# Kernel tuning notes

Measured on AMD Instinct MI355X. Metric: run time of the kernel, lower is better.

The kernel has to match this reference:

```python
import jax, jax.numpy as jnp
import numpy as np

B, T, D = 2, 2048, 2048
H = 16
SEM_HD, GEO_HD = 64, 64
SEM_D, GEO_D = H * SEM_HD, H * GEO_HD  # 1024, 1024
V_D = 2048
V_HD = V_D // H  # 128
ROPE_BASE = 10000.0
NEG_INF = -1e9


def _shape(x, hd):
    # (B, T, H*hd) -> (B, H, T, hd)
    b, t, _ = x.shape
    return x.reshape(b, t, H, hd).transpose(0, 2, 1, 3)


def _rope(x, pos_offset=0):
    # half-split (Llama-style) rotary on last dim; x: (B, H, T, hd)
    hd = x.shape[-1]
    half = hd // 2
    inv_freq = 1.0 / (ROPE_BASE ** (jnp.arange(0, half, dtype=jnp.float32) / half))
    pos = jnp.arange(x.shape[2], dtype=jnp.float32) + pos_offset
    ang = pos[:, None] * inv_freq[None, :]            # (T, half)
    cos, sin = jnp.cos(ang), jnp.sin(ang)
    x1, x2 = x[..., :half], x[..., half:]
    return jnp.concatenate([x1 * cos - x2 * sin, x2 * cos + x1 * sin], axis=-1).astype(x.dtype)


def setup_inputs() -> dict:
    key = jax.random.key(0)
    ks = jax.random.split(key, 9)
    s = lambda fan_in: 1.0 / np.sqrt(fan_in)
    return {
        "x": jax.random.normal(ks[0], (B, T, D), dtype=jnp.float32),
        "w_q_sem": jax.random.normal(ks[1], (D, SEM_D), dtype=jnp.float32) * s(D),
        "w_k_sem": jax.random.normal(ks[2], (D, SEM_D), dtype=jnp.float32) * s(D),
        "w_q_geo": jax.random.normal(ks[3], (D, GEO_D), dtype=jnp.float32) * s(D),
        "w_k_geo": jax.random.normal(ks[4], (D, GEO_D), dtype=jnp.float32) * s(D),
        "w_v": jax.random.normal(ks[5], (D, V_D), dtype=jnp.float32) * s(D),
        "w_out": jax.random.normal(ks[6], (V_D, D), dtype=jnp.float32) * s(V_D),
        "gate_logit": jax.random.normal(ks[7], (H,), dtype=jnp.float32) * 0.1,
        "gate_w": jax.random.normal(ks[8], (D, H), dtype=jnp.float32) * 0.01,
    }


def reference(x, w_q_sem, w_k_sem, w_q_geo, w_k_geo, w_v, w_out, gate_logit, gate_w):
    sem_scale = 1.0 / np.sqrt(float(SEM_HD))
    geo_scale = 1.0 / np.sqrt(float(GEO_HD))

    qs = _shape(x @ w_q_sem, SEM_HD)   # (B,H,T,sem_hd)
    ks = _shape(x @ w_k_sem, SEM_HD)
    qg = _shape(x @ w_q_geo, GEO_HD)   # (B,H,T,geo_hd)
    kg = _shape(x @ w_k_geo, GEO_HD)
    vh = _shape(x @ w_v, V_HD)         # (B,H,T,v_hd)

    # RoPE only on geometric dims
    qg = _rope(qg)
    kg = _rope(kg)

    sem_scores = jnp.einsum("bhtd,bhsd->bhts", qs, ks) * sem_scale
    geo_scores = jnp.einsum("bhtd,bhsd->bhts", qg, kg) * geo_scale

    # per-head gate: static logit + dynamic projection of x, sigmoid in fp32
    dyn = (x @ gate_w).transpose(0, 2, 1)[..., None]            # (B,H,T,1)
    gate = jax.nn.sigmoid(gate_logit[None, :, None, None] + dyn)
    scores = gate * sem_scores + (1.0 - gate) * geo_scores      # (B,H,T,S)

    causal = jnp.tril(jnp.ones((T, T), dtype=bool))
    scores = jnp.where(causal[None, None], scores, NEG_INF)
    attn = jax.nn.softmax(scores, axis=-1)

    out = jnp.einsum("bhts,bhsd->bhtd", attn, vh)               # (B,H,T,v_hd)
    y = out.transpose(0, 2, 1, 3).reshape(B, T, V_D) @ w_out    # (B,T,D)
    return y
```

## Files before the change

kernel.cpp:

```cpp
#include <hip/hip_runtime.h>
#include <hip/hip_bf16.h>
#include <math.h>

#define B_ 2
#define T_ 2048
#define D_ 2048
#define H_ 16

typedef __attribute__((ext_vector_type(8))) short bf16x8;
typedef __attribute__((ext_vector_type(4))) float f32x4;
typedef unsigned short ushort_t;

__device__ __forceinline__ ushort_t f2bf(float f) {
    unsigned int u = __float_as_uint(f);
    u += 0x7fffu + ((u >> 16) & 1u);
    return (ushort_t)(u >> 16);
}

__device__ __forceinline__ void gl_lds16(const void* g, void* l) {
    __builtin_amdgcn_global_load_lds(
        (const __attribute__((address_space(1))) void*)g,
        (__attribute__((address_space(3))) void*)l, 16, 0, 0);
}

__global__ __launch_bounds__(256) void cvt_bf16(
    const float* __restrict__ in, ushort_t* __restrict__ out)
{
    const int base = (blockIdx.x * 256 + threadIdx.x) * 8;
    const float4 a = *(const float4*)(in + base);
    const float4 b = *(const float4*)(in + base + 4);
    unsigned int r0 = (unsigned int)f2bf(a.x) | ((unsigned int)f2bf(a.y) << 16);
    unsigned int r1 = (unsigned int)f2bf(a.z) | ((unsigned int)f2bf(a.w) << 16);
    unsigned int r2 = (unsigned int)f2bf(b.x) | ((unsigned int)f2bf(b.y) << 16);
    unsigned int r3 = (unsigned int)f2bf(b.z) | ((unsigned int)f2bf(b.w) << 16);
    *(uint4*)(out + base) = make_uint4(r0, r1, r2, r3);
}

__global__ __launch_bounds__(256) void cvt_tr_bf16(
    const float* __restrict__ in, ushort_t* __restrict__ out, int K, int N)
{
    __shared__ float t[64][65];
    const int n0 = blockIdx.x * 64, k0 = blockIdx.y * 64;
    const int tx = threadIdx.x & 63, ty = threadIdx.x >> 6;
#pragma unroll
    for (int i = 0; i < 16; i++) {
        const int r = i * 4 + ty;
        t[r][tx] = in[(size_t)(k0 + r) * N + n0 + tx];
    }
    __syncthreads();
#pragma unroll
    for (int i = 0; i < 16; i++) {
        const int nn = i * 4 + ty;
        out[(size_t)(n0 + nn) * K + k0 + tx] = f2bf(t[tx][nn]);
    }
}

__device__ __forceinline__ void gemm_core(
    const ushort_t* __restrict__ Ab, const ushort_t* __restrict__ BTb,
    int K, int row0, int col0,
    ushort_t* As, ushort_t* Bs, f32x4 (&acc)[4][4], int w, int lane)
{
    const int lm = lane & 15, lk = (lane >> 4) << 3;
    const int wr = w >> 1, wc = w & 1;
#pragma unroll
    for (int m = 0; m < 4; m++)
#pragma unroll
        for (int n = 0; n < 4; n++) {
            acc[m][n][0] = 0.f; acc[m][n][1] = 0.f;
            acc[m][n][2] = 0.f; acc[m][n][3] = 0.f;
        }

    for (int k0 = 0; k0 < K; k0 += 32) {
        __syncthreads();
#pragma unroll
        for (int i = 0; i < 2; i++) {
            const int chunk = i * 4 + w;
            const int idx = chunk * 64 + lane;
            const int r = idx >> 2;
            const int c = (idx & 3) << 3;
            gl_lds16(Ab + (size_t)(row0 + r) * K + k0 + c, As + chunk * 512);
            gl_lds16(BTb + (size_t)(col0 + r) * K + k0 + c, Bs + chunk * 512);
        }
        __syncthreads();

        bf16x8 av[4], bv[4];
#pragma unroll
        for (int m = 0; m < 4; m++)
            av[m] = *(const bf16x8*)&As[(wr * 64 + m * 16 + lm) * 32 + lk];
#pragma unroll
        for (int n = 0; n < 4; n++)
            bv[n] = *(const bf16x8*)&Bs[(wc * 64 + n * 16 + lm) * 32 + lk];
#pragma unroll
        for (int m = 0; m < 4; m++)
#pragma unroll
            for (int n = 0; n < 4; n++)
                acc[m][n] = __builtin_amdgcn_mfma_f32_16x16x32_bf16(
                    av[m], bv[n], acc[m][n], 0, 0, 0);
    }
}

__device__ __forceinline__ void xcd_tile(int& row0, int& col0)
{
    const int o = blockIdx.y * gridDim.x + blockIdx.x;
    const int nwg = gridDim.x * gridDim.y;
    const int s = (o & 7) * (nwg >> 3) + (o >> 3);
    col0 = (s % gridDim.x) << 7;
    row0 = (s / gridDim.x) << 7;
}

__global__ __launch_bounds__(256) void gemm_bf16_bt(
    const ushort_t* __restrict__ Ab, const ushort_t* __restrict__ BTb,
    float* __restrict__ C, int N, int K)
{
    __shared__ ushort_t As[4096];
    __shared__ ushort_t Bs[4096];
    const int tid = threadIdx.x;
    const int w = tid >> 6, lane = tid & 63;
    int row0, col0;
    xcd_tile(row0, col0);
    f32x4 acc[4][4];
    gemm_core(Ab, BTb, K, row0, col0, As, Bs, acc, w, lane);

    const int wr = w >> 1, wc = w & 1;
    const int lm = lane & 15;
#pragma unroll
    for (int m = 0; m < 4; m++) {
        const int rowb = row0 + wr * 64 + m * 16 + ((lane >> 4) << 2);
#pragma unroll
        for (int n = 0; n < 4; n++) {
            const int col = col0 + wc * 64 + n * 16 + lm;
#pragma unroll
            for (int r = 0; r < 4; r++)
                C[(size_t)(rowb + r) * N + col] = acc[m][n][r];
        }
    }
}

__global__ __launch_bounds__(256) void gemm_bf16_bf16out(
    const ushort_t* __restrict__ Ab, const ushort_t* __restrict__ BTb,
    ushort_t* __restrict__ C, int N, int K)
{
    __shared__ ushort_t As[4096];
    __shared__ ushort_t Bs[4096];
    const int tid = threadIdx.x;
    const int w = tid >> 6, lane = tid & 63;
    int row0, col0;
    xcd_tile(row0, col0);
    f32x4 acc[4][4];
    gemm_core(Ab, BTb, K, row0, col0, As, Bs, acc, w, lane);

    const int wr = w >> 1, wc = w & 1;
    const int lm = lane & 15;
#pragma unroll
    for (int m = 0; m < 4; m++) {
        const int rowb = row0 + wr * 64 + m * 16 + ((lane >> 4) << 2);
#pragma unroll
        for (int n = 0; n < 4; n++) {
            const int col = col0 + wc * 64 + n * 16 + lm;
#pragma unroll
            for (int r = 0; r < 4; r++)
                C[(size_t)(rowb + r) * N + col] = f2bf(acc[m][n][r]);
        }
    }
}

__global__ __launch_bounds__(256) void gemm_qk_fused(
    const ushort_t* __restrict__ Ab, const ushort_t* __restrict__ BTb,
    const float* __restrict__ GATE, const float2* __restrict__ tab,
    ushort_t* __restrict__ Qb, ushort_t* __restrict__ Kb, int K)
{
    __shared__ ushort_t As[4096];
    __shared__ ushort_t Bs[4096];
    const int tid = threadIdx.x;
    const int w = tid >> 6, lane = tid & 63;
    int row0, col0;
    xcd_tile(row0, col0);
    f32x4 acc[4][4];
    gemm_core(Ab, BTb, K, row0, col0, As, Bs, acc, w, lane);

    const int wr = w >> 1, wc = w & 1;
    const int lm = lane & 15, lg = lane >> 4;
    const int col_base = col0 + wc * 64;
    const int region = col_base >> 10;
    const int h = (col_base >> 6) & 15;

#pragma unroll
    for (int m = 0; m < 4; m++) {
        const int rbase = row0 + wr * 64 + m * 16 + (lg << 2);
#pragma unroll
        for (int r = 0; r < 4; r++) {
            const int row = rbase + r;
            const int t = row & (T_ - 1);
            const int bq = row >> 11;
            const size_t obase = ((size_t)(bq * 16 + h) * 2048 + t) * 128;
            if (region == 0) {
                const float sc = GATE[row * 16 + h] * 0.125f;
#pragma unroll
                for (int n = 0; n < 4; n++)
                    Qb[obase + n * 16 + lm] = f2bf(acc[m][n][r] * sc);
            } else if (region == 1) {
                const int sw = (t & 7) << 3;
#pragma unroll
                for (int n = 0; n < 4; n++)
                    Kb[obase + ((n * 16 + lm) ^ sw)] = f2bf(acc[m][n][r]);
            } else if (region == 2) {
                const float sc = (1.f - GATE[row * 16 + h]) * 0.125f;
#pragma unroll
                for (int n = 0; n < 2; n++) {
                    const int j = n * 16 + lm;
                    const float2 cs = tab[t * 32 + j];
                    const float x1 = acc[m][n][r], x2 = acc[m][n + 2][r];
                    Qb[obase + 64 + j] = f2bf((x1 * cs.x - x2 * cs.y) * sc);
                    Qb[obase + 96 + j] = f2bf((x2 * cs.x + x1 * cs.y) * sc);
                }
            } else {
                const int sw = (t & 7) << 3;
#pragma unroll
                for (int n = 0; n < 2; n++) {
                    const int j = n * 16 + lm;
                    const float2 cs = tab[t * 32 + j];
                    const float x1 = acc[m][n][r], x2 = acc[m][n + 2][r];
                    Kb[obase + ((64 + j) ^ sw)] = f2bf(x1 * cs.x - x2 * cs.y);
                    Kb[obase + ((96 + j) ^ sw)] = f2bf(x2 * cs.x + x1 * cs.y);
                }
            }
        }
    }
}

__global__ __launch_bounds__(256) void gate_kernel(
    const float* __restrict__ x, const float* __restrict__ gw,
    const float* __restrict__ glogit, float* __restrict__ gate)
{
    __shared__ float xs[2048];
    __shared__ float red[256];
    const int row = blockIdx.x, tid = threadIdx.x;
#pragma unroll
    for (int i = 0; i < 8; i++) xs[i * 256 + tid] = x[(size_t)row * 2048 + i * 256 + tid];
    __syncthreads();
    const int h = tid & 15, chunk = tid >> 4;
    float acc = 0.f;
#pragma unroll 4
    for (int d0 = 0; d0 < 128; d0++) {
        const int d = chunk * 128 + d0;
        acc += xs[d] * gw[d * 16 + h];
    }
    red[tid] = acc;
    __syncthreads();
    for (int st = 8; st >= 1; st >>= 1) {
        if (chunk < st) red[chunk * 16 + h] += red[(chunk + st) * 16 + h];
        __syncthreads();
    }
    if (tid < 16) gate[row * 16 + tid] = 1.f / (1.f + expf(-(glogit[tid] + red[tid])));
}

__global__ __launch_bounds__(256) void rope_table(float2* __restrict__ tab)
{
    const int gid = blockIdx.x * 256 + threadIdx.x;
    const int j = gid & 31, t = gid >> 5;
    const float invf = exp2f((float)j * -0.41524101186091903f);
    const float ang = (float)t * invf;
    tab[gid] = make_float2(cosf(ang), sinf(ang));
}

__global__ __launch_bounds__(256) void prep_v(
    const ushort_t* __restrict__ Vbb, ushort_t* __restrict__ Vt)
{
    __shared__ ushort_t tile[64][65];
    const int t0 = blockIdx.x * 64, dv0 = blockIdx.y * 64, bh = blockIdx.z;
    const int b = bh >> 4, h = bh & 15;
    const int c = threadIdx.x & 63, rq = threadIdx.x >> 6;
#pragma unroll
    for (int i = 0; i < 16; i++) {
        const int r = i * 4 + rq;
        tile[r][c] = Vbb[(size_t)(b * T_ + t0 + r) * 2048 + h * 128 + dv0 + c];
    }
    __syncthreads();
#pragma unroll
    for (int i = 0; i < 16; i++) {
        const int dvr = i * 4 + rq;
        const int dv = dv0 + dvr;
        Vt[((size_t)bh * 128 + dv) * 2048 + t0 + (c ^ ((dv & 7) << 3))] = tile[c][dvr];
    }
}

__global__ __launch_bounds__(256, 2) void attn_mfma(
    const ushort_t* __restrict__ Qb, const ushort_t* __restrict__ Kb,
    const ushort_t* __restrict__ Vt, ushort_t* __restrict__ OUT)
{
    __shared__ ushort_t Ks[64 * 128];
    __shared__ ushort_t Vs[128 * 64];
    __shared__ ushort_t Ps[4][32 * 72];

    const int tid = threadIdx.x;
    const int w = tid >> 6, l = tid & 63;
    const int lg = l >> 4, lm = l & 15;
    const int bh = blockIdx.y;
    const int t0 = (gridDim.x - 1 - blockIdx.x) << 7;
    const size_t hb = (size_t)bh * 2048 * 128;

    bf16x8 qf[2][4];
#pragma unroll
    for (int m = 0; m < 2; m++)
#pragma unroll
        for (int ks = 0; ks < 4; ks++)
            qf[m][ks] = *(const bf16x8*)(Qb + hb +
                (size_t)(t0 + w * 32 + m * 16 + lm) * 128 + ks * 32 + lg * 8);

    f32x4 o[2][8];
    float mi[2][4], li[2][4];
#pragma unroll
    for (int m = 0; m < 2; m++) {
#pragma unroll
        for (int r = 0; r < 4; r++) { mi[m][r] = -1e30f; li[m][r] = 0.f; }
#pragma unroll
        for (int nv = 0; nv < 8; nv++) {
            o[m][nv][0] = 0.f; o[m][nv][1] = 0.f; o[m][nv][2] = 0.f; o[m][nv][3] = 0.f;
        }
    }

    ushort_t* pw = &Ps[w][0];
    const int nkt = (t0 >> 6) + 2;

    for (int kt = 0; kt < nkt; kt++) {
        const int s0 = kt << 6;
        __syncthreads();
#pragma unroll
        for (int rr = 0; rr < 4; rr++) {
            const int chunk = rr * 4 + w;
            gl_lds16(Kb + hb + (size_t)(s0 + chunk * 4 + lg) * 128 + lm * 8,
                     Ks + chunk * 512);
        }
#pragma unroll
        for (int rr = 0; rr < 4; rr++) {
            const int chunk = rr * 4 + w;
            gl_lds16(Vt + hb + (size_t)(chunk * 8 + (l >> 3)) * 2048 + s0 + (l & 7) * 8,
                     Vs + chunk * 512);
        }
        __syncthreads();

        f32x4 sacc[2][4];
#pragma unroll
        for (int m = 0; m < 2; m++)
#pragma unroll
            for (int n = 0; n < 4; n++) {
                sacc[m][n][0] = 0.f; sacc[m][n][1] = 0.f;
                sacc[m][n][2] = 0.f; sacc[m][n][3] = 0.f;
            }
#pragma unroll
        for (int ks = 0; ks < 4; ks++) {
            bf16x8 bfr[4];
#pragma unroll
            for (int n = 0; n < 4; n++) {
                const int key = n * 16 + lm;
                const int d = ks * 32 + lg * 8;
                bfr[n] = *(const bf16x8*)&Ks[key * 128 + (d ^ ((key & 7) << 3))];
            }
#pragma unroll
            for (int m = 0; m < 2; m++)
#pragma unroll
                for (int n = 0; n < 4; n++)
                    sacc[m][n] = __builtin_amdgcn_mfma_f32_16x16x32_bf16(
                        qf[m][ks], bfr[n], sacc[m][n], 0, 0, 0);
        }

        if (kt >= nkt - 2) {
#pragma unroll
            for (int m = 0; m < 2; m++)
#pragma unroll
                for (int n = 0; n < 4; n++)
#pragma unroll
                    for (int r = 0; r < 4; r++) {
                        const int rowt = t0 + w * 32 + m * 16 + lg * 4 + r;
                        const int colt = s0 + n * 16 + lm;
                        if (colt > rowt) sacc[m][n][r] = -1e30f;
                    }
        }

#pragma unroll
        for (int m = 0; m < 2; m++) {
#pragma unroll
            for (int r = 0; r < 4; r++) {
                float mt = fmaxf(fmaxf(sacc[m][0][r], sacc[m][1][r]),
                                 fmaxf(sacc[m][2][r], sacc[m][3][r]));
                mt = fmaxf(mt, __shfl_xor(mt, 1));
                mt = fmaxf(mt, __shfl_xor(mt, 2));
                mt = fmaxf(mt, __shfl_xor(mt, 4));
                mt = fmaxf(mt, __shfl_xor(mt, 8));
                const float mnew = fmaxf(mi[m][r], mt);
                const float alpha = __expf(mi[m][r] - mnew);
                float rs = 0.f;
#pragma unroll
                for (int n = 0; n < 4; n++) {
                    const float p = __expf(sacc[m][n][r] - mnew);
                    sacc[m][n][r] = p;
                    rs += p;
                }
                rs += __shfl_xor(rs, 1);
                rs += __shfl_xor(rs, 2);
                rs += __shfl_xor(rs, 4);
                rs += __shfl_xor(rs, 8);
                li[m][r] = li[m][r] * alpha + rs;
                mi[m][r] = mnew;
#pragma unroll
                for (int nv = 0; nv < 8; nv++) o[m][nv][r] *= alpha;
#pragma unroll
                for (int n = 0; n < 4; n++)
                    pw[(m * 16 + lg * 4 + r) * 72 + n * 16 + lm] = f2bf(sacc[m][n][r]);
            }
        }

#pragma unroll
        for (int ks2 = 0; ks2 < 2; ks2++) {
            bf16x8 pa[2];
#pragma unroll
            for (int m = 0; m < 2; m++)
                pa[m] = *(const bf16x8*)&pw[(m * 16 + lm) * 72 + ks2 * 32 + lg * 8];
#pragma unroll
            for (int nv = 0; nv < 8; nv++) {
                const int dv = nv * 16 + lm;
                const bf16x8 vb = *(const bf16x8*)&Vs[dv * 64 +
                    ((ks2 * 32 + lg * 8) ^ ((dv & 7) << 3))];
#pragma unroll
                for (int m = 0; m < 2; m++)
                    o[m][nv] = __builtin_amdgcn_mfma_f32_16x16x32_bf16(
                        pa[m], vb, o[m][nv], 0, 0, 0);
            }
        }
    }

    const int b = bh >> 4, h = bh & 15;
#pragma unroll
    for (int m = 0; m < 2; m++)
#pragma unroll
        for (int r = 0; r < 4; r++) {
            const float inv = 1.f / li[m][r];
            const int trow = t0 + w * 32 + m * 16 + lg * 4 + r;
            ushort_t* orow = OUT + (size_t)(b * T_ + trow) * 2048 + h * 128 + lm;
#pragma unroll
            for (int nv = 0; nv < 8; nv++)
                orow[nv * 16] = f2bf(o[m][nv][r] * inv);
        }
}

extern "C" void kernel_launch(void* const* d_in, const int* in_sizes, int n_in,
                              void* d_out, int out_size, void* d_ws, size_t ws_size,
                              hipStream_t stream)
{
    const float* x       = (const float*)d_in[0];
    const float* w_q_sem = (const float*)d_in[1];
    const float* w_k_sem = (const float*)d_in[2];
    const float* w_q_geo = (const float*)d_in[3];
    const float* w_k_geo = (const float*)d_in[4];
    const float* w_v     = (const float*)d_in[5];
    const float* w_out   = (const float*)d_in[6];
    const float* glogit  = (const float*)d_in[7];
    const float* gw      = (const float*)d_in[8];
    float* out = (float*)d_out;

    const int M = B_ * T_;
    const size_t MB8 = (size_t)8 * 1024 * 1024;

    ushort_t* xbf = (ushort_t*)d_ws;
    ushort_t* WT  = xbf + MB8;
    ushort_t* Qb  = WT + MB8;
    ushort_t* Kb  = Qb + MB8;
    ushort_t* Vt  = Kb + MB8;
    ushort_t* Vbb = Vt + MB8;
    float* GATE   = (float*)(Vbb + MB8);
    float2* TAB   = (float2*)(GATE + 65536);
    ushort_t* ATTbf = Vbb;

    dim3 blk(256);

    cvt_bf16<<<dim3(M * 2048 / (256 * 8)), blk, 0, stream>>>(x, xbf);
    cvt_tr_bf16<<<dim3(16, 32), blk, 0, stream>>>(w_q_sem, WT + (size_t)0 * 2097152, 2048, 1024);
    cvt_tr_bf16<<<dim3(16, 32), blk, 0, stream>>>(w_k_sem, WT + (size_t)1 * 2097152, 2048, 1024);
    cvt_tr_bf16<<<dim3(16, 32), blk, 0, stream>>>(w_q_geo, WT + (size_t)2 * 2097152, 2048, 1024);
    cvt_tr_bf16<<<dim3(16, 32), blk, 0, stream>>>(w_k_geo, WT + (size_t)3 * 2097152, 2048, 1024);
    gate_kernel<<<dim3(M), blk, 0, stream>>>(x, gw, glogit, GATE);
    rope_table<<<dim3(256), blk, 0, stream>>>(TAB);

    gemm_qk_fused<<<dim3(32, 32), blk, 0, stream>>>(xbf, WT, GATE, TAB, Qb, Kb, 2048);

    cvt_tr_bf16<<<dim3(32, 32), blk, 0, stream>>>(w_v, WT, 2048, 2048);
    gemm_bf16_bf16out<<<dim3(16, 32), blk, 0, stream>>>(xbf, WT, Vbb, 2048, 2048);
    prep_v<<<dim3(T_ / 64, 2, 32), blk, 0, stream>>>(Vbb, Vt);

    attn_mfma<<<dim3(T_ / 128, 32), blk, 0, stream>>>(Qb, Kb, Vt, ATTbf);

    cvt_tr_bf16<<<dim3(32, 32), blk, 0, stream>>>(w_out, WT, 2048, 2048);
    gemm_bf16_bt<<<dim3(16, 32), blk, 0, stream>>>(ATTbf, WT, out, 2048, 2048);
}
```

Baseline: 552.2 us.

## Fuse prep kernels, pair causal tiles in attention, add lazy rescale and setprio

```diff
diff --git a/kernel.cpp b/kernel.cpp
--- a/kernel.cpp
+++ b/kernel.cpp
@@ -23,17 +23,49 @@
         (__attribute__((address_space(3))) void*)l, 16, 0, 0);
 }
 
-__global__ __launch_bounds__(256) void cvt_bf16(
-    const float* __restrict__ in, ushort_t* __restrict__ out)
-{
-    const int base = (blockIdx.x * 256 + threadIdx.x) * 8;
-    const float4 a = *(const float4*)(in + base);
-    const float4 b = *(const float4*)(in + base + 4);
+__global__ __launch_bounds__(256) void cvt_gate_kernel(
+    const float* __restrict__ x, const float* __restrict__ gw,
+    const float* __restrict__ glogit,
+    ushort_t* __restrict__ xbf, float* __restrict__ gate)
+{
+    __shared__ float xs[2048];
+    __shared__ float red[256];
+    const int row = blockIdx.x, tid = threadIdx.x;
+
+    const float4 a = *(const float4*)(x + (size_t)row * 2048 + tid * 8);
+    const float4 b = *(const float4*)(x + (size_t)row * 2048 + tid * 8 + 4);
     unsigned int r0 = (unsigned int)f2bf(a.x) | ((unsigned int)f2bf(a.y) << 16);
     unsigned int r1 = (unsigned int)f2bf(a.z) | ((unsigned int)f2bf(a.w) << 16);
     unsigned int r2 = (unsigned int)f2bf(b.x) | ((unsigned int)f2bf(b.y) << 16);
     unsigned int r3 = (unsigned int)f2bf(b.z) | ((unsigned int)f2bf(b.w) << 16);
-    *(uint4*)(out + base) = make_uint4(r0, r1, r2, r3);
+    *(uint4*)(xbf + (size_t)row * 2048 + tid * 8) = make_uint4(r0, r1, r2, r3);
+    *(float4*)&xs[tid * 8] = a;
+    *(float4*)&xs[tid * 8 + 4] = b;
+    __syncthreads();
+
+    const int h = tid & 15, chunk = tid >> 4;
+    float acc = 0.f;
+#pragma unroll 4
+    for (int d0 = 0; d0 < 128; d0++) {
+        const int d = chunk * 128 + d0;
+        acc += xs[d] * gw[d * 16 + h];
+    }
+    red[tid] = acc;
+    __syncthreads();
+    for (int st = 8; st >= 1; st >>= 1) {
+        if (chunk < st) red[chunk * 16 + h] += red[(chunk + st) * 16 + h];
+        __syncthreads();
+    }
+    if (tid < 16) gate[row * 16 + tid] = 1.f / (1.f + expf(-(glogit[tid] + red[tid])));
+}
+
+__global__ __launch_bounds__(256) void rope_table(float2* __restrict__ tab)
+{
+    const int gid = blockIdx.x * 256 + threadIdx.x;
+    const int j = gid & 31, t = gid >> 5;
+    const float invf = exp2f((float)j * -0.41524101186091903f);
+    const float ang = (float)t * invf;
+    tab[gid] = make_float2(cosf(ang), sinf(ang));
 }
 
 __global__ __launch_bounds__(256) void cvt_tr_bf16(
@@ -52,6 +84,31 @@
     for (int i = 0; i < 16; i++) {
         const int nn = i * 4 + ty;
         out[(size_t)(n0 + nn) * K + k0 + tx] = f2bf(t[tx][nn]);
+    }
+}
+
+__global__ __launch_bounds__(256) void cvt_tr4_bf16(
+    const float* __restrict__ s0, const float* __restrict__ s1,
+    const float* __restrict__ s2, const float* __restrict__ s3,
+    ushort_t* __restrict__ out)
+{
+    __shared__ float t[64][65];
+    const int z = blockIdx.z;
+    const float* in = (z == 0) ? s0 : (z == 1) ? s1 : (z == 2) ? s2 : s3;
+    ushort_t* o = out + (size_t)z * 2097152;
+    const int N = 1024, K = 2048;
+    const int n0 = blockIdx.x * 64, k0 = blockIdx.y * 64;
+    const int tx = threadIdx.x & 63, ty = threadIdx.x >> 6;
+#pragma unroll
+    for (int i = 0; i < 16; i++) {
+        const int r = i * 4 + ty;
+        t[r][tx] = in[(size_t)(k0 + r) * N + n0 + tx];
+    }
+    __syncthreads();
+#pragma unroll
+    for (int i = 0; i < 16; i++) {
+        const int nn = i * 4 + ty;
+        o[(size_t)(n0 + nn) * K + k0 + tx] = f2bf(t[tx][nn]);
     }
 }
 
@@ -90,12 +147,14 @@
 #pragma unroll
         for (int n = 0; n < 4; n++)
             bv[n] = *(const bf16x8*)&Bs[(wc * 64 + n * 16 + lm) * 32 + lk];
+        __builtin_amdgcn_s_setprio(1);
 #pragma unroll
         for (int m = 0; m < 4; m++)
 #pragma unroll
             for (int n = 0; n < 4; n++)
                 acc[m][n] = __builtin_amdgcn_mfma_f32_16x16x32_bf16(
                     av[m], bv[n], acc[m][n], 0, 0, 0);
+        __builtin_amdgcn_s_setprio(0);
     }
 }
 
@@ -228,41 +287,6 @@
     }
 }
 
-__global__ __launch_bounds__(256) void gate_kernel(
-    const float* __restrict__ x, const float* __restrict__ gw,
-    const float* __restrict__ glogit, float* __restrict__ gate)
-{
-    __shared__ float xs[2048];
-    __shared__ float red[256];
-    const int row = blockIdx.x, tid = threadIdx.x;
-#pragma unroll
-    for (int i = 0; i < 8; i++) xs[i * 256 + tid] = x[(size_t)row * 2048 + i * 256 + tid];
-    __syncthreads();
-    const int h = tid & 15, chunk = tid >> 4;
-    float acc = 0.f;
-#pragma unroll 4
-    for (int d0 = 0; d0 < 128; d0++) {
-        const int d = chunk * 128 + d0;
-        acc += xs[d] * gw[d * 16 + h];
-    }
-    red[tid] = acc;
-    __syncthreads();
-    for (int st = 8; st >= 1; st >>= 1) {
-        if (chunk < st) red[chunk * 16 + h] += red[(chunk + st) * 16 + h];
-        __syncthreads();
-    }
-    if (tid < 16) gate[row * 16 + tid] = 1.f / (1.f + expf(-(glogit[tid] + red[tid])));
-}
-
-__global__ __launch_bounds__(256) void rope_table(float2* __restrict__ tab)
-{
-    const int gid = blockIdx.x * 256 + threadIdx.x;
-    const int j = gid & 31, t = gid >> 5;
-    const float invf = exp2f((float)j * -0.41524101186091903f);
-    const float ang = (float)t * invf;
-    tab[gid] = make_float2(cosf(ang), sinf(ang));
-}
-
 __global__ __launch_bounds__(256) void prep_v(
     const ushort_t* __restrict__ Vbb, ushort_t* __restrict__ Vt)
 {
@@ -296,151 +320,164 @@
     const int w = tid >> 6, l = tid & 63;
     const int lg = l >> 4, lm = l & 15;
     const int bh = blockIdx.y;
-    const int t0 = (gridDim.x - 1 - blockIdx.x) << 7;
+    const int pair = blockIdx.x;
     const size_t hb = (size_t)bh * 2048 * 128;
-
-    bf16x8 qf[2][4];
-#pragma unroll
-    for (int m = 0; m < 2; m++)
-#pragma unroll
-        for (int ks = 0; ks < 4; ks++)
-            qf[m][ks] = *(const bf16x8*)(Qb + hb +
-                (size_t)(t0 + w * 32 + m * 16 + lm) * 128 + ks * 32 + lg * 8);
-
-    f32x4 o[2][8];
-    float mi[2][4], li[2][4];
-#pragma unroll
-    for (int m = 0; m < 2; m++) {
-#pragma unroll
-        for (int r = 0; r < 4; r++) { mi[m][r] = -1e30f; li[m][r] = 0.f; }
-#pragma unroll
-        for (int nv = 0; nv < 8; nv++) {
-            o[m][nv][0] = 0.f; o[m][nv][1] = 0.f; o[m][nv][2] = 0.f; o[m][nv][3] = 0.f;
-        }
-    }
-
+    const int b = bh >> 4, h = bh & 15;
     ushort_t* pw = &Ps[w][0];
-    const int nkt = (t0 >> 6) + 2;
-
-    for (int kt = 0; kt < nkt; kt++) {
-        const int s0 = kt << 6;
-        __syncthreads();
-#pragma unroll
-        for (int rr = 0; rr < 4; rr++) {
-            const int chunk = rr * 4 + w;
-            gl_lds16(Kb + hb + (size_t)(s0 + chunk * 4 + lg) * 128 + lm * 8,
-                     Ks + chunk * 512);
-        }
-#pragma unroll
-        for (int rr = 0; rr < 4; rr++) {
-            const int chunk = rr * 4 + w;
-            gl_lds16(Vt + hb + (size_t)(chunk * 8 + (l >> 3)) * 2048 + s0 + (l & 7) * 8,
-                     Vs + chunk * 512);
-        }
-        __syncthreads();
-
-        f32x4 sacc[2][4];
+
+    for (int half = 0; half < 2; half++) {
+        const int tile = (half == 0) ? (15 - pair) : pair;
+        const int t0 = tile << 7;
+
+        bf16x8 qf[2][4];
 #pragma unroll
         for (int m = 0; m < 2; m++)
 #pragma unroll
-            for (int n = 0; n < 4; n++) {
-                sacc[m][n][0] = 0.f; sacc[m][n][1] = 0.f;
-                sacc[m][n][2] = 0.f; sacc[m][n][3] = 0.f;
-            }
-#pragma unroll
-        for (int ks = 0; ks < 4; ks++) {
-            bf16x8 bfr[4];
-#pragma unroll
-            for (int n = 0; n < 4; n++) {
-                const int key = n * 16 + lm;
-                const int d = ks * 32 + lg * 8;
-                bfr[n] = *(const bf16x8*)&Ks[key * 128 + (d ^ ((key & 7) << 3))];
-            }
+            for (int ks = 0; ks < 4; ks++)
+                qf[m][ks] = *(const bf16x8*)(Qb + hb +
+                    (size_t)(t0 + w * 32 + m * 16 + lm) * 128 + ks * 32 + lg * 8);
+
+        f32x4 o[2][8];
+        float mi[2][4], li[2][4];
+#pragma unroll
+        for (int m = 0; m < 2; m++) {
+#pragma unroll
+            for (int r = 0; r < 4; r++) { mi[m][r] = -1e30f; li[m][r] = 0.f; }
+#pragma unroll
+            for (int nv = 0; nv < 8; nv++) {
+                o[m][nv][0] = 0.f; o[m][nv][1] = 0.f;
+                o[m][nv][2] = 0.f; o[m][nv][3] = 0.f;
+            }
+        }
+
+        const int nkt = 2 * tile + 2;
+        for (int kt = 0; kt < nkt; kt++) {
+            const int s0 = kt << 6;
+            __syncthreads();
+#pragma unroll
+            for (int rr = 0; rr < 4; rr++) {
+                const int chunk = rr * 4 + w;
+                gl_lds16(Kb + hb + (size_t)(s0 + chunk * 4 + lg) * 128 + lm * 8,
+                         Ks + chunk * 512);
+            }
+#pragma unroll
+            for (int rr = 0; rr < 4; rr++) {
+                const int chunk = rr * 4 + w;
+                gl_lds16(Vt + hb + (size_t)(chunk * 8 + (l >> 3)) * 2048 + s0 + (l & 7) * 8,
+                         Vs + chunk * 512);
+            }
+            __syncthreads();
+
+            f32x4 sacc[2][4];
 #pragma unroll
             for (int m = 0; m < 2; m++)
 #pragma unroll
-                for (int n = 0; n < 4; n++)
-                    sacc[m][n] = __builtin_amdgcn_mfma_f32_16x16x32_bf16(
-                        qf[m][ks], bfr[n], sacc[m][n], 0, 0, 0);
-        }
-
-        if (kt >= nkt - 2) {
-#pragma unroll
-            for (int m = 0; m < 2; m++)
-#pragma unroll
-                for (int n = 0; n < 4; n++)
-#pragma unroll
-                    for (int r = 0; r < 4; r++) {
-                        const int rowt = t0 + w * 32 + m * 16 + lg * 4 + r;
-                        const int colt = s0 + n * 16 + lm;
-                        if (colt > rowt) sacc[m][n][r] = -1e30f;
+                for (int n = 0; n < 4; n++) {
+                    sacc[m][n][0] = 0.f; sacc[m][n][1] = 0.f;
+                    sacc[m][n][2] = 0.f; sacc[m][n][3] = 0.f;
+                }
+#pragma unroll
+            for (int ks = 0; ks < 4; ks++) {
+                bf16x8 bfr[4];
+#pragma unroll
+                for (int n = 0; n < 4; n++) {
+                    const int key = n * 16 + lm;
+                    const int d = ks * 32 + lg * 8;
+                    bfr[n] = *(const bf16x8*)&Ks[key * 128 + (d ^ ((key & 7) << 3))];
+                }
+                __builtin_amdgcn_s_setprio(1);
+#pragma unroll
+                for (int m = 0; m < 2; m++)
+#pragma unroll
+                    for (int n = 0; n < 4; n++)
+                        sacc[m][n] = __builtin_amdgcn_mfma_f32_16x16x32_bf16(
+                            qf[m][ks], bfr[n], sacc[m][n], 0, 0, 0);
+                __builtin_amdgcn_s_setprio(0);
+            }
+
+            if (kt >= nkt - 2) {
+#pragma unroll
+                for (int m = 0; m < 2; m++)
+#pragma unroll
+                    for (int n = 0; n < 4; n++)
+#pragma unroll
+                        for (int r = 0; r < 4; r++) {
+                            const int rowt = t0 + w * 32 + m * 16 + lg * 4 + r;
+                            const int colt = s0 + n * 16 + lm;
+                            if (colt > rowt) sacc[m][n][r] = -1e30f;
+                        }
+            }
+
+#pragma unroll
+            for (int m = 0; m < 2; m++) {
+#pragma unroll
+                for (int r = 0; r < 4; r++) {
+                    float mt = fmaxf(fmaxf(sacc[m][0][r], sacc[m][1][r]),
+                                     fmaxf(sacc[m][2][r], sacc[m][3][r]));
+                    mt = fmaxf(mt, __shfl_xor(mt, 1));
+                    mt = fmaxf(mt, __shfl_xor(mt, 2));
+                    mt = fmaxf(mt, __shfl_xor(mt, 4));
+                    mt = fmaxf(mt, __shfl_xor(mt, 8));
+                    const float miold = mi[m][r];
+                    if (mt > miold + 8.f) {
+                        const float alpha = __expf(miold - mt);
+                        li[m][r] *= alpha;
+#pragma unroll
+                        for (int nv = 0; nv < 8; nv++) o[m][nv][r] *= alpha;
+                        mi[m][r] = mt;
                     }
-        }
-
-#pragma unroll
-        for (int m = 0; m < 2; m++) {
+                    const float mcur = mi[m][r];
+                    float rs = 0.f;
+#pragma unroll
+                    for (int n = 0; n < 4; n++) {
+                        const float p = __expf(sacc[m][n][r] - mcur);
+                        sacc[m][n][r] = p;
+                        rs += p;
+                    }
+                    rs += __shfl_xor(rs, 1);
+                    rs += __shfl_xor(rs, 2);
+                    rs += __shfl_xor(rs, 4);
+                    rs += __shfl_xor(rs, 8);
+                    li[m][r] += rs;
+#pragma unroll
+                    for (int n = 0; n < 4; n++)
+                        pw[(m * 16 + lg * 4 + r) * 72 + n * 16 + lm] = f2bf(sacc[m][n][r]);
+                }
+            }
+
+#pragma unroll
+            for (int ks2 = 0; ks2 < 2; ks2++) {
+                bf16x8 pa[2];
+#pragma unroll
+                for (int m = 0; m < 2; m++)
+                    pa[m] = *(const bf16x8*)&pw[(m * 16 + lm) * 72 + ks2 * 32 + lg * 8];
+                __builtin_amdgcn_s_setprio(1);
+#pragma unroll
+                for (int nv = 0; nv < 8; nv++) {
+                    const int dv = nv * 16 + lm;
+                    const bf16x8 vb = *(const bf16x8*)&Vs[dv * 64 +
+                        ((ks2 * 32 + lg * 8) ^ ((dv & 7) << 3))];
+#pragma unroll
+                    for (int m = 0; m < 2; m++)
+                        o[m][nv] = __builtin_amdgcn_mfma_f32_16x16x32_bf16(
+                            pa[m], vb, o[m][nv], 0, 0, 0);
+                }
+                __builtin_amdgcn_s_setprio(0);
+            }
+        }
+
+#pragma unroll
+        for (int m = 0; m < 2; m++)
 #pragma unroll
             for (int r = 0; r < 4; r++) {
-                float mt = fmaxf(fmaxf(sacc[m][0][r], sacc[m][1][r]),
-                                 fmaxf(sacc[m][2][r], sacc[m][3][r]));
-                mt = fmaxf(mt, __shfl_xor(mt, 1));
-                mt = fmaxf(mt, __shfl_xor(mt, 2));
-                mt = fmaxf(mt, __shfl_xor(mt, 4));
-                mt = fmaxf(mt, __shfl_xor(mt, 8));
-                const float mnew = fmaxf(mi[m][r], mt);
-                const float alpha = __expf(mi[m][r] - mnew);
-                float rs = 0.f;
-#pragma unroll
-                for (int n = 0; n < 4; n++) {
-                    const float p = __expf(sacc[m][n][r] - mnew);
-                    sacc[m][n][r] = p;
-                    rs += p;
-                }
-                rs += __shfl_xor(rs, 1);
-                rs += __shfl_xor(rs, 2);
-                rs += __shfl_xor(rs, 4);
-                rs += __shfl_xor(rs, 8);
-                li[m][r] = li[m][r] * alpha + rs;
-                mi[m][r] = mnew;
-#pragma unroll
-                for (int nv = 0; nv < 8; nv++) o[m][nv][r] *= alpha;
-#pragma unroll
-                for (int n = 0; n < 4; n++)
-                    pw[(m * 16 + lg * 4 + r) * 72 + n * 16 + lm] = f2bf(sacc[m][n][r]);
-            }
-        }
-
-#pragma unroll
-        for (int ks2 = 0; ks2 < 2; ks2++) {
-            bf16x8 pa[2];
-#pragma unroll
-            for (int m = 0; m < 2; m++)
-                pa[m] = *(const bf16x8*)&pw[(m * 16 + lm) * 72 + ks2 * 32 + lg * 8];
-#pragma unroll
-            for (int nv = 0; nv < 8; nv++) {
-                const int dv = nv * 16 + lm;
-                const bf16x8 vb = *(const bf16x8*)&Vs[dv * 64 +
-                    ((ks2 * 32 + lg * 8) ^ ((dv & 7) << 3))];
-#pragma unroll
-                for (int m = 0; m < 2; m++)
-                    o[m][nv] = __builtin_amdgcn_mfma_f32_16x16x32_bf16(
-                        pa[m], vb, o[m][nv], 0, 0, 0);
-            }
-        }
-    }
-
-    const int b = bh >> 4, h = bh & 15;
-#pragma unroll
-    for (int m = 0; m < 2; m++)
-#pragma unroll
-        for (int r = 0; r < 4; r++) {
-            const float inv = 1.f / li[m][r];
-            const int trow = t0 + w * 32 + m * 16 + lg * 4 + r;
-            ushort_t* orow = OUT + (size_t)(b * T_ + trow) * 2048 + h * 128 + lm;
-#pragma unroll
-            for (int nv = 0; nv < 8; nv++)
-                orow[nv * 16] = f2bf(o[m][nv][r] * inv);
-        }
+                const float inv = 1.f / li[m][r];
+                const int trow = t0 + w * 32 + m * 16 + lg * 4 + r;
+                ushort_t* orow = OUT + (size_t)(b * T_ + trow) * 2048 + h * 128 + lm;
+#pragma unroll
+                for (int nv = 0; nv < 8; nv++)
+                    orow[nv * 16] = f2bf(o[m][nv][r] * inv);
+            }
+    }
 }
 
 extern "C" void kernel_launch(void* const* d_in, const int* in_sizes, int n_in,
@@ -473,13 +510,9 @@
 
     dim3 blk(256);
 
-    cvt_bf16<<<dim3(M * 2048 / (256 * 8)), blk, 0, stream>>>(x, xbf);
-    cvt_tr_bf16<<<dim3(16, 32), blk, 0, stream>>>(w_q_sem, WT + (size_t)0 * 2097152, 2048, 1024);
-    cvt_tr_bf16<<<dim3(16, 32), blk, 0, stream>>>(w_k_sem, WT + (size_t)1 * 2097152, 2048, 1024);
-    cvt_tr_bf16<<<dim3(16, 32), blk, 0, stream>>>(w_q_geo, WT + (size_t)2 * 2097152, 2048, 1024);
-    cvt_tr_bf16<<<dim3(16, 32), blk, 0, stream>>>(w_k_geo, WT + (size_t)3 * 2097152, 2048, 1024);
-    gate_kernel<<<dim3(M), blk, 0, stream>>>(x, gw, glogit, GATE);
+    cvt_gate_kernel<<<dim3(M), blk, 0, stream>>>(x, gw, glogit, xbf, GATE);
     rope_table<<<dim3(256), blk, 0, stream>>>(TAB);
+    cvt_tr4_bf16<<<dim3(16, 32, 4), blk, 0, stream>>>(w_q_sem, w_k_sem, w_q_geo, w_k_geo, WT);
 
     gemm_qk_fused<<<dim3(32, 32), blk, 0, stream>>>(xbf, WT, GATE, TAB, Qb, Kb, 2048);
 
@@ -487,7 +520,7 @@
     gemm_bf16_bf16out<<<dim3(16, 32), blk, 0, stream>>>(xbf, WT, Vbb, 2048, 2048);
     prep_v<<<dim3(T_ / 64, 2, 32), blk, 0, stream>>>(Vbb, Vt);
 
-    attn_mfma<<<dim3(T_ / 128, 32), blk, 0, stream>>>(Qb, Kb, Vt, ATTbf);
+    attn_mfma<<<dim3(8, 32), blk, 0, stream>>>(Qb, Kb, Vt, ATTbf);
 
     cvt_tr_bf16<<<dim3(32, 32), blk, 0, stream>>>(w_out, WT, 2048, 2048);
     gemm_bf16_bt<<<dim3(16, 32), blk, 0, stream>>>(ATTbf, WT, out, 2048, 2048);
```

Measured after the change: 557.4 us. No clear change (+0.9%).
